# Optimization experiments

Hardware: AMD Instinct MI355X
Metric: run time of the kernel (lower is better)

Reference implementation:

```python
import jax, jax.numpy as jnp
import numpy as np

HEADS = 8
DIM_HEAD = 64
QUERY_DIM = 512
CONTEXT_DIM = 768
INNER_DIM = HEADS * DIM_HEAD  # 512
SCALE = DIM_HEAD ** -0.5


def setup_inputs() -> dict:
    key = jax.random.key(0)
    ks = jax.random.split(key, 7)
    B, N, M = 4, 2048, 1024
    x = jax.random.normal(ks[0], (B, N, QUERY_DIM), dtype=jnp.float32)
    context = jax.random.normal(ks[1], (B, M, CONTEXT_DIM), dtype=jnp.float32)
    # torch Linear weights stored as (out_features, in_features); y = x @ W.T
    Wq = jax.random.normal(ks[2], (INNER_DIM, QUERY_DIM), dtype=jnp.float32) * (QUERY_DIM ** -0.5)
    Wk = jax.random.normal(ks[3], (INNER_DIM, CONTEXT_DIM), dtype=jnp.float32) * (CONTEXT_DIM ** -0.5)
    Wv = jax.random.normal(ks[4], (INNER_DIM, CONTEXT_DIM), dtype=jnp.float32) * (CONTEXT_DIM ** -0.5)
    Wo = jax.random.normal(ks[5], (QUERY_DIM, INNER_DIM), dtype=jnp.float32) * (INNER_DIM ** -0.5)
    bo = jax.random.normal(ks[6], (QUERY_DIM,), dtype=jnp.float32) * 0.01
    return {"x": x, "context": context, "Wq": Wq, "Wk": Wk, "Wv": Wv, "Wo": Wo, "bo": bo}


def reference(x, context, Wq, Wk, Wv, Wo, bo):
    B, N, _ = x.shape
    M = context.shape[1]
    h, d = HEADS, DIM_HEAD
    q = jnp.einsum('bnc,ic->bni', x, Wq)        # [B,N,inner]
    k = jnp.einsum('bmc,ic->bmi', context, Wk)  # [B,M,inner]
    v = jnp.einsum('bmc,ic->bmi', context, Wv)  # [B,M,inner]
    # split heads: b n (h d) -> b h n d
    q = q.reshape(B, N, h, d).transpose(0, 2, 1, 3)
    k = k.reshape(B, M, h, d).transpose(0, 2, 1, 3)
    v = v.reshape(B, M, h, d).transpose(0, 2, 1, 3)
    # fp32 upcast for QK^T (inputs already fp32; kept explicit for fidelity)
    sim = jnp.einsum('bhnd,bhmd->bhnm', q.astype(jnp.float32), k.astype(jnp.float32)) * SCALE
    attn = jax.nn.softmax(sim, axis=-1)
    out = jnp.einsum('bhnm,bhmd->bhnd', attn, v)  # [B,h,N,d]
    out = out.transpose(0, 2, 1, 3).reshape(B, N, h * d)  # b n (h d)
    return jnp.einsum('bni,oi->bno', out, Wo) + bo  # dropout p=0 in eval
```

## Files before the change

### kernel.cpp

```cpp
#include <hip/hip_runtime.h>

using u16 = unsigned short;
typedef __bf16 bf16x8 __attribute__((ext_vector_type(8)));
typedef __bf16 bf16x2 __attribute__((ext_vector_type(2)));
typedef float  f32x4  __attribute__((ext_vector_type(4)));
typedef float  f32x16 __attribute__((ext_vector_type(16)));

#define MFMA16x16x32 __builtin_amdgcn_mfma_f32_16x16x32_bf16
#define MFMA32x32x16 __builtin_amdgcn_mfma_f32_32x32x16_bf16

#if __has_builtin(__builtin_amdgcn_exp2f)
#define EXP2 __builtin_amdgcn_exp2f
#else
#define EXP2 exp2f
#endif

static __device__ __forceinline__ unsigned f2bf_u(float f){
  unsigned x = __builtin_bit_cast(unsigned, f);
  return (x + 0x7fffu + ((x >> 16) & 1u)) >> 16;
}

static __device__ __forceinline__ void gll16(const void* g, void* l){
  __builtin_amdgcn_global_load_lds((const __attribute__((address_space(1))) void*)g,
                                   (__attribute__((address_space(3))) void*)l, 16, 0, 0);
}

static __device__ __forceinline__ f32x16 splat16(float x){
  f32x16 v;
#pragma unroll
  for (int i = 0; i < 16; ++i) v[i] = x;
  return v;
}

__global__ void __launch_bounds__(256) cvt_all(
    const float* __restrict__ x,  u16* __restrict__ xb,
    const float* __restrict__ cx, u16* __restrict__ cxb,
    const float* __restrict__ wq, u16* __restrict__ wqb,
    const float* __restrict__ wk, u16* __restrict__ wkb,
    const float* __restrict__ wv, u16* __restrict__ wvb,
    const float* __restrict__ wo, u16* __restrict__ wob)
{
  const float* in; u16* out; int n4;
  switch (blockIdx.y){
    case 0: in=x;  out=xb;  n4=(4*2048*512)/4; break;
    case 1: in=cx; out=cxb; n4=(4*1024*768)/4; break;
    case 2: in=wq; out=wqb; n4=(512*512)/4;    break;
    case 3: in=wk; out=wkb; n4=(512*768)/4;    break;
    case 4: in=wv; out=wvb; n4=(512*768)/4;    break;
    default:in=wo; out=wob; n4=(512*512)/4;    break;
  }
  int i = blockIdx.x*256 + threadIdx.x;
  const int stride = gridDim.x*256;
  for (; i < n4; i += stride){
    float4 f = ((const float4*)in)[i];
    ushort4 u;
    u.x = (u16)f2bf_u(f.x); u.y = (u16)f2bf_u(f.y);
    u.z = (u16)f2bf_u(f.z); u.w = (u16)f2bf_u(f.w);
    ((ushort4*)out)[i] = u;
  }
}

template<int LDA, int LDB, int KK, int OM>
static __device__ __forceinline__ void gemm_tile64(
    const u16* __restrict__ Ap, const u16* __restrict__ Bp,
    void* __restrict__ Cv, int ldc, int bx, int by,
    const float* __restrict__ bias, float scale,
    u16* __restrict__ sAp, u16* __restrict__ sBp)
{
  const int tid = threadIdx.x;
  const int w = tid >> 6, lane = tid & 63;
  const int wr = w >> 1, wc = w & 1;
  const long tm = (long)bx * 128;
  const long tn = (long)by * 64;

  f32x4 acc[4][2] = {};

  const int srl = lane >> 3, scc = lane & 7;

  auto stage = [&](int kt, int bb){
#pragma unroll
    for (int i = 0; i < 4; ++i){
      const int row = w*32 + i*8 + srl;
      const int sw = scc ^ (row & 7);
      gll16(Ap + (tm + row)*LDA + kt*64 + sw*8, sAp + bb*(128*64) + (w*32 + i*8)*64);
    }
#pragma unroll
    for (int i = 0; i < 2; ++i){
      const int row = w*16 + i*8 + srl;
      const int sw = scc ^ (row & 7);
      gll16(Bp + (tn + row)*LDB + kt*64 + sw*8, sBp + bb*(64*64) + (w*16 + i*8)*64);
    }
  };

  const int fr = lane & 15, fg = lane >> 4;
  constexpr int NK = KK / 64;

  stage(0, 0);
  __syncthreads();
  for (int kt = 0; kt < NK; ++kt){
    if (kt + 1 < NK) stage(kt + 1, (kt + 1) & 1);
    const int bb = kt & 1;
    bf16x8 af[4][2], bfr[2][2];
#pragma unroll
    for (int fm = 0; fm < 4; ++fm){
      const int row = wr*64 + fm*16 + fr;
      const int swz = row & 7;
#pragma unroll
      for (int s = 0; s < 2; ++s)
        af[fm][s] = *(const bf16x8*)&sAp[bb*(128*64) + row*64 + ((s*4 + fg) ^ swz)*8];
    }
#pragma unroll
    for (int fn = 0; fn < 2; ++fn){
      const int row = wc*32 + fn*16 + fr;
      const int swz = row & 7;
#pragma unroll
      for (int s = 0; s < 2; ++s)
        bfr[fn][s] = *(const bf16x8*)&sBp[bb*(64*64) + row*64 + ((s*4 + fg) ^ swz)*8];
    }
#pragma unroll
    for (int s = 0; s < 2; ++s)
#pragma unroll
      for (int fm = 0; fm < 4; ++fm)
#pragma unroll
        for (int fn = 0; fn < 2; ++fn)
          acc[fm][fn] = MFMA16x16x32(af[fm][s], bfr[fn][s], acc[fm][fn], 0, 0, 0);
    __syncthreads();
  }

#pragma unroll
  for (int fm = 0; fm < 4; ++fm){
#pragma unroll
    for (int fn = 0; fn < 2; ++fn){
      const long row0 = tm + wr*64 + fm*16 + fg*4;
      const long col  = tn + wc*32 + fn*16 + fr;
      if (OM == 0){
        u16* C = (u16*)Cv;
#pragma unroll
        for (int rr = 0; rr < 4; ++rr)
          C[(row0 + rr)*ldc + col] = (u16)f2bf_u(acc[fm][fn][rr] * scale);
      } else {
        float* C = (float*)Cv;
        const float bv = bias[col];
#pragma unroll
        for (int rr = 0; rr < 4; ++rr)
          C[(row0 + rr)*ldc + col] = acc[fm][fn][rr] + bv;
      }
    }
  }
}

template<int LDA, int LDB, int KK, int OM>
static __device__ __forceinline__ void gemm_tile128(
    const u16* __restrict__ Ap, const u16* __restrict__ Bp,
    void* __restrict__ Cv, int ldc, int bx, int by,
    const float* __restrict__ bias, float scale,
    u16* __restrict__ sAp, u16* __restrict__ sBp)
{
  const int tid = threadIdx.x;
  const int w = tid >> 6, lane = tid & 63;
  const int wr = w >> 1, wc = w & 1;
  const long tm = (long)bx * 128;
  const long tn = (long)by * 128;

  f32x4 acc[4][4] = {};

  const int srl = lane >> 3, scc = lane & 7;

  auto stage = [&](int kt, int bb){
#pragma unroll
    for (int i = 0; i < 4; ++i){
      const int row = w*32 + i*8 + srl;
      const int sw = scc ^ (row & 7);
      gll16(Ap + (tm + row)*LDA + kt*64 + sw*8, sAp + bb*(128*64) + (w*32 + i*8)*64);
      gll16(Bp + (tn + row)*LDB + kt*64 + sw*8, sBp + bb*(128*64) + (w*32 + i*8)*64);
    }
  };

  const int fr = lane & 15, fg = lane >> 4;
  constexpr int NK = KK / 64;

  stage(0, 0);
  __syncthreads();
  for (int kt = 0; kt < NK; ++kt){
    if (kt + 1 < NK) stage(kt + 1, (kt + 1) & 1);
    const int bb = kt & 1;
    bf16x8 af[4][2], bfr[4][2];
#pragma unroll
    for (int fm = 0; fm < 4; ++fm){
      const int row = wr*64 + fm*16 + fr;
      const int swz = row & 7;
#pragma unroll
      for (int s = 0; s < 2; ++s)
        af[fm][s] = *(const bf16x8*)&sAp[bb*(128*64) + row*64 + ((s*4 + fg) ^ swz)*8];
    }
#pragma unroll
    for (int fn = 0; fn < 4; ++fn){
      const int row = wc*64 + fn*16 + fr;
      const int swz = row & 7;
#pragma unroll
      for (int s = 0; s < 2; ++s)
        bfr[fn][s] = *(const bf16x8*)&sBp[bb*(128*64) + row*64 + ((s*4 + fg) ^ swz)*8];
    }
#pragma unroll
    for (int s = 0; s < 2; ++s)
#pragma unroll
      for (int fm = 0; fm < 4; ++fm)
#pragma unroll
        for (int fn = 0; fn < 4; ++fn)
          acc[fm][fn] = MFMA16x16x32(af[fm][s], bfr[fn][s], acc[fm][fn], 0, 0, 0);
    __syncthreads();
  }

#pragma unroll
  for (int fm = 0; fm < 4; ++fm){
#pragma unroll
    for (int fn = 0; fn < 4; ++fn){
      const long row0 = tm + wr*64 + fm*16 + fg*4;
      const long col  = tn + wc*64 + fn*16 + fr;
      if (OM == 0){
        u16* C = (u16*)Cv;
#pragma unroll
        for (int rr = 0; rr < 4; ++rr)
          C[(row0 + rr)*ldc + col] = (u16)f2bf_u(acc[fm][fn][rr] * scale);
      } else {
        float* C = (float*)Cv;
        const float bv = bias[col];
#pragma unroll
        for (int rr = 0; rr < 4; ++rr)
          C[(row0 + rr)*ldc + col] = acc[fm][fn][rr] + bv;
      }
    }
  }
}

__global__ __launch_bounds__(256, 2) void proj_fused(
    const u16* __restrict__ xb,  const u16* __restrict__ cxb,
    const u16* __restrict__ wqb, const u16* __restrict__ wkb,
    const u16* __restrict__ wvb,
    u16* __restrict__ qb, u16* __restrict__ kb, u16* __restrict__ vtb,
    float qscale)
{
  __shared__ u16 sA[2*128*64];
  __shared__ u16 sB[2*128*64];
  const int bid = blockIdx.x;
  const int lid = (bid & 7)*64 + (bid >> 3);
  if (lid < 256){
    gemm_tile128<512,512,512,0>(xb, wqb, (void*)qb, 512, lid >> 2, lid & 3,
                                nullptr, qscale, sA, sB);
  } else if (lid < 384){
    const int t = lid - 256;
    gemm_tile128<768,768,768,0>(cxb, wkb, (void*)kb, 512, t >> 2, t & 3,
                                nullptr, 1.0f, sA, sB);
  } else {
    const int t = lid - 384, z = t >> 5, r = t & 31;
    gemm_tile128<768,768,768,0>(wvb, cxb + (long)z*1024*768,
                                (void*)(vtb + (long)z*512*1024), 1024,
                                r >> 3, r & 7, nullptr, 1.0f, sA, sB);
  }
}

__global__ __launch_bounds__(256, 3) void gemm_out(
    const u16* __restrict__ ab, const u16* __restrict__ wob,
    float* __restrict__ out, const float* __restrict__ bias)
{
  __shared__ u16 sA[2*128*64];
  __shared__ u16 sB[2*64*64];
  const int bid = blockIdx.x;
  const int lid = (bid & 7)*64 + (bid >> 3);
  gemm_tile64<512,512,512,1>(ab, wob, (void*)out, 512, lid >> 3, lid & 7,
                             bias, 1.0f, sA, sB);
}

__global__ __launch_bounds__(512, 2) void attn_fwd(
    const u16* __restrict__ Q,
    const u16* __restrict__ Kb,
    const u16* __restrict__ Vt,
    u16* __restrict__ O)
{
  const int bid = blockIdx.x;
  const int lid = (bid & 7)*32 + (bid >> 3);
  const int qx = lid & 7, hh = (lid >> 3) & 7, b = lid >> 6;
  const int w = threadIdx.x >> 6, lane = threadIdx.x & 63;
  const int q31 = lane & 31, hi = lane >> 5;
  const int w4 = w & 3, kvg = w >> 2;
  const int q0 = qx*256 + w4*64;

  __shared__ u16 sAll[8][8192];
  __shared__ float sLsP[16*32];
  __shared__ float sLsT[8*32];

  bf16x8 qf[2][4];
#pragma unroll
  for (int j = 0; j < 2; ++j){
    const u16* qrow = Q + (long)(b*2048 + q0 + j*32 + q31)*512 + hh*64;
#pragma unroll
    for (int ks = 0; ks < 4; ++ks)
      qf[j][ks] = *(const bf16x8*)(qrow + ks*16 + hi*8);
  }

  f32x16 o[2][2] = {{splat16(0.f), splat16(0.f)}, {splat16(0.f), splat16(0.f)}};
  float lsum0 = 0.f, lsum1 = 0.f;

  const int srl = lane >> 3, scc = lane & 7;
  const int vr4 = lane >> 4, vc16 = lane & 15;

  auto stage = [&](int t){
    const int tv = 2*t + kvg;
    const int sl = t & 1;
#pragma unroll
    for (int i = 0; i < 4; ++i){
      const int row = w4*32 + i*8 + srl;
      const int cs = scc ^ (row & 7);
      gll16(Kb + (long)(b*1024 + tv*128 + row)*512 + hh*64 + cs*8,
            &sAll[kvg*2 + sl][(w4*32 + i*8)*64]);
    }
#pragma unroll
    for (int i = 0; i < 4; ++i){
      const int d = w4*16 + i*4 + vr4;
      const int cs = vc16 ^ (d & 15);
      gll16(Vt + (long)(b*512 + hh*64 + d)*1024 + tv*128 + cs*8,
            &sAll[4 + kvg*2 + sl][(w4*16 + i*4)*128]);
    }
  };

  stage(0);

  for (int t = 0; t < 4; ++t){
    asm volatile("s_waitcnt vmcnt(0)" ::: "memory");
    __builtin_amdgcn_s_barrier();
    asm volatile("" ::: "memory");
    if (t + 1 < 4) stage(t + 1);

    const u16* sKp = sAll[kvg*2 + (t & 1)];
    const u16* sVp = sAll[4 + kvg*2 + (t & 1)];

#pragma unroll
    for (int mt = 0; mt < 4; ++mt){
      f32x16 s0 = splat16(-16.f), s1 = splat16(-16.f);
      const int row = mt*32 + q31;
      const int swz = row & 7;
      __builtin_amdgcn_s_setprio(1);
#pragma unroll
      for (int ks = 0; ks < 4; ++ks){
        bf16x8 kf = *(const bf16x8*)&sKp[row*64 + ((ks*2 + hi) ^ swz)*8];
        s0 = MFMA32x32x16(kf, qf[0][ks], s0, 0, 0, 0);
        s1 = MFMA32x32x16(kf, qf[1][ks], s1, 0, 0, 0);
      }
      __builtin_amdgcn_s_setprio(0);

#pragma unroll
      for (int r = 0; r < 16; ++r) s0[r] = EXP2(s0[r]);
#pragma unroll
      for (int r = 0; r < 16; ++r) s1[r] = EXP2(s1[r]);
      {
        float a0=s0[0]+s0[1], a1=s0[2]+s0[3], a2=s0[4]+s0[5], a3=s0[6]+s0[7];
        float a4=s0[8]+s0[9], a5=s0[10]+s0[11], a6=s0[12]+s0[13], a7=s0[14]+s0[15];
        lsum0 += ((a0+a1)+(a2+a3)) + ((a4+a5)+(a6+a7));
        float c0=s1[0]+s1[1], c1=s1[2]+s1[3], c2=s1[4]+s1[5], c3=s1[6]+s1[7];
        float c4=s1[8]+s1[9], c5=s1[10]+s1[11], c6=s1[12]+s1[13], c7=s1[14]+s1[15];
        lsum1 += ((c0+c1)+(c2+c3)) + ((c4+c5)+(c6+c7));
      }
      unsigned pk0[8], pk1[8];
#pragma unroll
      for (int p2 = 0; p2 < 8; ++p2){
        union { bf16x2 h; unsigned u; } t0, t1;
        t0.h[0] = (__bf16)s0[2*p2]; t0.h[1] = (__bf16)s0[2*p2 + 1]; pk0[p2] = t0.u;
        t1.h[0] = (__bf16)s1[2*p2]; t1.h[1] = (__bf16)s1[2*p2 + 1]; pk1[p2] = t1.u;
      }

#pragma unroll
      for (int sl2 = 0; sl2 < 2; ++sl2){
        union { unsigned u[4]; bf16x8 v; } pa0, pa1;
        {
          unsigned a = pk0[sl2*4 + 0], bq = pk0[sl2*4 + 2];
          asm volatile("v_permlane32_swap_b32 %0, %1" : "+v"(a), "+v"(bq));
          pa0.u[0] = a;  pa0.u[2] = bq;
          unsigned a2 = pk0[sl2*4 + 1], b2 = pk0[sl2*4 + 3];
          asm volatile("v_permlane32_swap_b32 %0, %1" : "+v"(a2), "+v"(b2));
          pa0.u[1] = a2; pa0.u[3] = b2;
        }
        {
          unsigned a = pk1[sl2*4 + 0], bq = pk1[sl2*4 + 2];
          asm volatile("v_permlane32_swap_b32 %0, %1" : "+v"(a), "+v"(bq));
          pa1.u[0] = a;  pa1.u[2] = bq;
          unsigned a2 = pk1[sl2*4 + 1], b2 = pk1[sl2*4 + 3];
          asm volatile("v_permlane32_swap_b32 %0, %1" : "+v"(a2), "+v"(b2));
          pa1.u[1] = a2; pa1.u[3] = b2;
        }
        const int s = mt*2 + sl2;
        __builtin_amdgcn_s_setprio(1);
#pragma unroll
        for (int fd = 0; fd < 2; ++fd){
          const int vrow = fd*32 + q31;
          bf16x8 bv = *(const bf16x8*)&sVp[vrow*128 + (((s*2 + hi) ^ (vrow & 15)))*8];
          o[0][fd] = MFMA32x32x16(pa0.v, bv, o[0][fd], 0, 0, 0);
          o[1][fd] = MFMA32x32x16(pa1.v, bv, o[1][fd], 0, 0, 0);
        }
        __builtin_amdgcn_s_setprio(0);
      }
    }
    asm volatile("" ::: "memory");
  }

  lsum0 += __shfl_xor(lsum0, 32);
  lsum1 += __shfl_xor(lsum1, 32);
  sLsP[(w*2 + 0)*32 + q31] = lsum0;
  sLsP[(w*2 + 1)*32 + q31] = lsum1;
  __syncthreads();

  float* sO = (float*)&sAll[0][0];
  if (w >= 4){
#pragma unroll
    for (int j = 0; j < 2; ++j){
#pragma unroll
      for (int fd = 0; fd < 2; ++fd){
        float* p = sO + ((((w - 4)*2 + j)*2 + fd)*64*20) + lane*20;
#pragma unroll
        for (int k = 0; k < 4; ++k){
          f32x4 t4;
#pragma unroll
          for (int e = 0; e < 4; ++e) t4[e] = o[j][fd][4*k + e];
          *(f32x4*)(p + 4*k) = t4;
        }
      }
    }
  }
  __syncthreads();

  if (w < 4){
#pragma unroll
    for (int j = 0; j < 2; ++j){
#pragma unroll
      for (int fd = 0; fd < 2; ++fd){
        const float* p = sO + (((w*2 + j)*2 + fd)*64*20) + lane*20;
#pragma unroll
        for (int k = 0; k < 4; ++k){
          f32x4 t4 = *(const f32x4*)(p + 4*k);
#pragma unroll
          for (int e = 0; e < 4; ++e) o[j][fd][4*k + e] += t4[e];
        }
      }
    }
    const float lt0 = lsum0 + sLsP[((w + 4)*2 + 0)*32 + q31];
    const float lt1 = lsum1 + sLsP[((w + 4)*2 + 1)*32 + q31];
    sLsT[(w*2 + 0)*32 + q31] = lt0;
    sLsT[(w*2 + 1)*32 + q31] = lt1;
  }
  __syncthreads();

  if (w < 4){
#pragma unroll
    for (int j = 0; j < 2; ++j){
      f32x4 inv[4];
#pragma unroll
      for (int g = 0; g < 4; ++g){
        f32x4 ls = *(const f32x4*)&sLsT[(w*2 + j)*32 + 8*g + 4*hi];
#pragma unroll
        for (int e = 0; e < 4; ++e) inv[g][e] = 1.0f / ls[e];
      }
      u16* orow = O + (long)(b*2048 + q0 + j*32)*512 + hh*64;
#pragma unroll
      for (int fd = 0; fd < 2; ++fd){
#pragma unroll
        for (int r = 0; r < 16; ++r){
          const int q = (r & 3) + 8*(r >> 2) + 4*hi;
          const float val = o[j][fd][r] * inv[r >> 2][r & 3];
          orow[(long)q*512 + fd*32 + q31] = (u16)f2bf_u(val);
        }
      }
    }
  }
}

extern "C" void kernel_launch(void* const* d_in, const int* in_sizes, int n_in,
                              void* d_out, int out_size, void* d_ws, size_t ws_size,
                              hipStream_t stream)
{
  (void)in_sizes; (void)n_in; (void)out_size; (void)ws_size;
  const float* x   = (const float*)d_in[0];
  const float* ctx = (const float*)d_in[1];
  const float* Wq  = (const float*)d_in[2];
  const float* Wk  = (const float*)d_in[3];
  const float* Wv  = (const float*)d_in[4];
  const float* Wo  = (const float*)d_in[5];
  const float* bo  = (const float*)d_in[6];
  float* out = (float*)d_out;

  char* ws = (char*)d_ws;
  u16* xb  = (u16*)(ws + 0);
  u16* cxb = (u16*)(ws + 8388608);
  u16* wqb = (u16*)(ws + 14680064);
  u16* wkb = (u16*)(ws + 15204352);
  u16* wvb = (u16*)(ws + 15990784);
  u16* wob = (u16*)(ws + 16777216);
  u16* qb  = (u16*)(ws + 17301504);
  u16* kb  = (u16*)(ws + 25690112);
  u16* vtb = (u16*)(ws + 29884416);
  u16* ab  = (u16*)(ws + 34078720);

  cvt_all<<<dim3(1024, 6, 1), 256, 0, stream>>>(x, xb, ctx, cxb, Wq, wqb,
                                                Wk, wkb, Wv, wvb, Wo, wob);

  proj_fused<<<dim3(512, 1, 1), 256, 0, stream>>>(
      xb, cxb, wqb, wkb, wvb, qb, kb, vtb, 0.18033688011112042f);

  attn_fwd<<<dim3(256, 1, 1), 512, 0, stream>>>(qb, kb, vtb, ab);

  gemm_out<<<dim3(512, 1, 1), 256, 0, stream>>>(ab, wob, out, bo);
}
```

Before: 66.82 us.

## Write K/V in MFMA-fragment order and load attention operands directly from global

The K and V projection epilogues now scatter their outputs into a pre-swizzled layout that matches the per-lane MFMA operand order. The attention kernel then reads K and V fragments straight from global memory into registers with coalesced 16-byte loads, with no LDS staging, barriers or double buffering. This removes LDS traffic and synchronisation in the attention loop. In exchange it gives up cross-wave data sharing through LDS, so every wave reissues its own global or L2 loads and memory latency is exposed to the MFMA chain. The projection stores also become scattered.

```diff
diff --git a/kernel.cpp b/kernel.cpp
--- a/kernel.cpp
+++ b/kernel.cpp
@@ -222,12 +222,37 @@
 #pragma unroll
         for (int rr = 0; rr < 4; ++rr)
           C[(row0 + rr)*ldc + col] = (u16)f2bf_u(acc[fm][fn][rr] * scale);
-      } else {
+      } else if (OM == 1){
         float* C = (float*)Cv;
         const float bv = bias[col];
 #pragma unroll
         for (int rr = 0; rr < 4; ++rr)
           C[(row0 + rr)*ldc + col] = acc[fm][fn][rr] + bv;
+      } else if (OM == 2){
+        u16* C = (u16*)Cv;
+        const int hh2 = (int)(col >> 6), d = (int)(col & 63);
+        const int ks = d >> 4, hi2 = (d >> 3) & 1, e = d & 7;
+#pragma unroll
+        for (int rr = 0; rr < 4; ++rr){
+          const long r = row0 + rr;
+          const int b2 = (int)(r >> 10), m = (int)(r & 1023);
+          const int tv = m >> 7, mtq = (m >> 5) & 3, q31r = m & 31;
+          const long off = ((long)((((b2*8 + hh2)*8 + tv)*4 + mtq)*4 + ks))*512
+                         + (hi2*32 + q31r)*8 + e;
+          C[off] = (u16)f2bf_u(acc[fm][fn][rr] * scale);
+        }
+      } else {
+        u16* C = (u16*)Cv;
+        const int m = (int)col;
+        const int tv = m >> 7, s = (m >> 4) & 7, hi2 = (m >> 3) & 1, e = m & 7;
+#pragma unroll
+        for (int rr = 0; rr < 4; ++rr){
+          const int i = (int)(row0 + rr);
+          const int hh2 = i >> 6, d0 = i & 63, fd = d0 >> 5, q31v = d0 & 31;
+          const long off = ((long)((((hh2*8 + tv)*8 + s)*2 + fd)*2 + hi2))*256
+                         + q31v*8 + e;
+          C[off] = (u16)f2bf_u(acc[fm][fn][rr] * scale);
+        }
       }
     }
   }
@@ -237,7 +262,7 @@
     const u16* __restrict__ xb,  const u16* __restrict__ cxb,
     const u16* __restrict__ wqb, const u16* __restrict__ wkb,
     const u16* __restrict__ wvb,
-    u16* __restrict__ qb, u16* __restrict__ kb, u16* __restrict__ vtb,
+    u16* __restrict__ qb, u16* __restrict__ kpb, u16* __restrict__ vpb,
     float qscale)
 {
   __shared__ u16 sA[2*128*64];
@@ -249,12 +274,12 @@
                                 nullptr, qscale, sA, sB);
   } else if (lid < 384){
     const int t = lid - 256;
-    gemm_tile128<768,768,768,0>(cxb, wkb, (void*)kb, 512, t >> 2, t & 3,
+    gemm_tile128<768,768,768,2>(cxb, wkb, (void*)kpb, 0, t >> 2, t & 3,
                                 nullptr, 1.0f, sA, sB);
   } else {
     const int t = lid - 384, z = t >> 5, r = t & 31;
-    gemm_tile128<768,768,768,0>(wvb, cxb + (long)z*1024*768,
-                                (void*)(vtb + (long)z*512*1024), 1024,
+    gemm_tile128<768,768,768,3>(wvb, cxb + (long)z*1024*768,
+                                (void*)(vpb + (long)z*524288), 0,
                                 r >> 3, r & 7, nullptr, 1.0f, sA, sB);
   }
 }
@@ -273,8 +298,8 @@
 
 __global__ __launch_bounds__(512, 2) void attn_fwd(
     const u16* __restrict__ Q,
-    const u16* __restrict__ Kb,
-    const u16* __restrict__ Vt,
+    const u16* __restrict__ Kp,
+    const u16* __restrict__ Vp,
     u16* __restrict__ O)
 {
   const int bid = blockIdx.x;
@@ -284,11 +309,15 @@
   const int q31 = lane & 31, hi = lane >> 5;
   const int w4 = w & 3, kvg = w >> 2;
   const int q0 = qx*256 + w4*64;
-
-  __shared__ u16 sAll[8][8192];
+  const int bh = b*8 + hh;
+
+  __shared__ float sO[4*2*2*1280];
   __shared__ float sLsP[16*32];
   __shared__ float sLsT[8*32];
 
+  const u16* Kb2 = Kp + (long)bh*65536 + lane*8;
+  const u16* Vb2 = Vp + (long)bh*65536 + lane*8;
+
   bf16x8 qf[2][4];
 #pragma unroll
   for (int j = 0; j < 2; ++j){
@@ -301,105 +330,81 @@
   f32x16 o[2][2] = {{splat16(0.f), splat16(0.f)}, {splat16(0.f), splat16(0.f)}};
   float lsum0 = 0.f, lsum1 = 0.f;
 
-  const int srl = lane >> 3, scc = lane & 7;
-  const int vr4 = lane >> 4, vc16 = lane & 15;
-
-  auto stage = [&](int t){
-    const int tv = 2*t + kvg;
-    const int sl = t & 1;
-#pragma unroll
-    for (int i = 0; i < 4; ++i){
-      const int row = w4*32 + i*8 + srl;
-      const int cs = scc ^ (row & 7);
-      gll16(Kb + (long)(b*1024 + tv*128 + row)*512 + hh*64 + cs*8,
-            &sAll[kvg*2 + sl][(w4*32 + i*8)*64]);
-    }
-#pragma unroll
-    for (int i = 0; i < 4; ++i){
-      const int d = w4*16 + i*4 + vr4;
-      const int cs = vc16 ^ (d & 15);
-      gll16(Vt + (long)(b*512 + hh*64 + d)*1024 + tv*128 + cs*8,
-            &sAll[4 + kvg*2 + sl][(w4*16 + i*4)*128]);
-    }
-  };
-
-  stage(0);
-
-  for (int t = 0; t < 4; ++t){
-    asm volatile("s_waitcnt vmcnt(0)" ::: "memory");
-    __builtin_amdgcn_s_barrier();
-    asm volatile("" ::: "memory");
-    if (t + 1 < 4) stage(t + 1);
-
-    const u16* sKp = sAll[kvg*2 + (t & 1)];
-    const u16* sVp = sAll[4 + kvg*2 + (t & 1)];
-
-#pragma unroll
-    for (int mt = 0; mt < 4; ++mt){
-      f32x16 s0 = splat16(-16.f), s1 = splat16(-16.f);
-      const int row = mt*32 + q31;
-      const int swz = row & 7;
+#pragma unroll 2
+  for (int u = 0; u < 16; ++u){
+    const int tv = kvg*4 + (u >> 2);
+    const int mt = u & 3;
+    const u16* kp = Kb2 + (long)((tv*4 + mt)*4)*512;
+    bf16x8 kf0 = *(const bf16x8*)(kp);
+    bf16x8 kf1 = *(const bf16x8*)(kp + 512);
+    bf16x8 kf2 = *(const bf16x8*)(kp + 1024);
+    bf16x8 kf3 = *(const bf16x8*)(kp + 1536);
+    const u16* vp = Vb2 + (long)((tv*8 + mt*2)*2)*512;
+    bf16x8 bv00 = *(const bf16x8*)(vp);
+    bf16x8 bv01 = *(const bf16x8*)(vp + 512);
+    bf16x8 bv10 = *(const bf16x8*)(vp + 1024);
+    bf16x8 bv11 = *(const bf16x8*)(vp + 1536);
+
+    f32x16 s0 = splat16(-16.f), s1 = splat16(-16.f);
+    __builtin_amdgcn_s_setprio(1);
+    s0 = MFMA32x32x16(kf0, qf[0][0], s0, 0, 0, 0);
+    s1 = MFMA32x32x16(kf0, qf[1][0], s1, 0, 0, 0);
+    s0 = MFMA32x32x16(kf1, qf[0][1], s0, 0, 0, 0);
+    s1 = MFMA32x32x16(kf1, qf[1][1], s1, 0, 0, 0);
+    s0 = MFMA32x32x16(kf2, qf[0][2], s0, 0, 0, 0);
+    s1 = MFMA32x32x16(kf2, qf[1][2], s1, 0, 0, 0);
+    s0 = MFMA32x32x16(kf3, qf[0][3], s0, 0, 0, 0);
+    s1 = MFMA32x32x16(kf3, qf[1][3], s1, 0, 0, 0);
+    __builtin_amdgcn_s_setprio(0);
+
+#pragma unroll
+    for (int r = 0; r < 16; ++r) s0[r] = EXP2(s0[r]);
+#pragma unroll
+    for (int r = 0; r < 16; ++r) s1[r] = EXP2(s1[r]);
+    {
+      float a0=s0[0]+s0[1], a1=s0[2]+s0[3], a2=s0[4]+s0[5], a3=s0[6]+s0[7];
+      float a4=s0[8]+s0[9], a5=s0[10]+s0[11], a6=s0[12]+s0[13], a7=s0[14]+s0[15];
+      lsum0 += ((a0+a1)+(a2+a3)) + ((a4+a5)+(a6+a7));
+      float c0=s1[0]+s1[1], c1=s1[2]+s1[3], c2=s1[4]+s1[5], c3=s1[6]+s1[7];
+      float c4=s1[8]+s1[9], c5=s1[10]+s1[11], c6=s1[12]+s1[13], c7=s1[14]+s1[15];
+      lsum1 += ((c0+c1)+(c2+c3)) + ((c4+c5)+(c6+c7));
+    }
+    unsigned pk0[8], pk1[8];
+#pragma unroll
+    for (int p2 = 0; p2 < 8; ++p2){
+      union { bf16x2 h; unsigned u; } t0, t1;
+      t0.h[0] = (__bf16)s0[2*p2]; t0.h[1] = (__bf16)s0[2*p2 + 1]; pk0[p2] = t0.u;
+      t1.h[0] = (__bf16)s1[2*p2]; t1.h[1] = (__bf16)s1[2*p2 + 1]; pk1[p2] = t1.u;
+    }
+
+#pragma unroll
+    for (int sl2 = 0; sl2 < 2; ++sl2){
+      union { unsigned u[4]; bf16x8 v; } pa0, pa1;
+      {
+        unsigned a = pk0[sl2*4 + 0], bq = pk0[sl2*4 + 2];
+        asm volatile("v_permlane32_swap_b32 %0, %1" : "+v"(a), "+v"(bq));
+        pa0.u[0] = a;  pa0.u[2] = bq;
+        unsigned a2 = pk0[sl2*4 + 1], b2 = pk0[sl2*4 + 3];
+        asm volatile("v_permlane32_swap_b32 %0, %1" : "+v"(a2), "+v"(b2));
+        pa0.u[1] = a2; pa0.u[3] = b2;
+      }
+      {
+        unsigned a = pk1[sl2*4 + 0], bq = pk1[sl2*4 + 2];
+        asm volatile("v_permlane32_swap_b32 %0, %1" : "+v"(a), "+v"(bq));
+        pa1.u[0] = a;  pa1.u[2] = bq;
+        unsigned a2 = pk1[sl2*4 + 1], b2 = pk1[sl2*4 + 3];
+        asm volatile("v_permlane32_swap_b32 %0, %1" : "+v"(a2), "+v"(b2));
+        pa1.u[1] = a2; pa1.u[3] = b2;
+      }
+      const bf16x8 bvf0 = sl2 ? bv10 : bv00;
+      const bf16x8 bvf1 = sl2 ? bv11 : bv01;
       __builtin_amdgcn_s_setprio(1);
-#pragma unroll
-      for (int ks = 0; ks < 4; ++ks){
-        bf16x8 kf = *(const bf16x8*)&sKp[row*64 + ((ks*2 + hi) ^ swz)*8];
-        s0 = MFMA32x32x16(kf, qf[0][ks], s0, 0, 0, 0);
-        s1 = MFMA32x32x16(kf, qf[1][ks], s1, 0, 0, 0);
-      }
+      o[0][0] = MFMA32x32x16(pa0.v, bvf0, o[0][0], 0, 0, 0);
+      o[1][0] = MFMA32x32x16(pa1.v, bvf0, o[1][0], 0, 0, 0);
+      o[0][1] = MFMA32x32x16(pa0.v, bvf1, o[0][1], 0, 0, 0);
+      o[1][1] = MFMA32x32x16(pa1.v, bvf1, o[1][1], 0, 0, 0);
       __builtin_amdgcn_s_setprio(0);
-
-#pragma unroll
-      for (int r = 0; r < 16; ++r) s0[r] = EXP2(s0[r]);
-#pragma unroll
-      for (int r = 0; r < 16; ++r) s1[r] = EXP2(s1[r]);
-      {
-        float a0=s0[0]+s0[1], a1=s0[2]+s0[3], a2=s0[4]+s0[5], a3=s0[6]+s0[7];
-        float a4=s0[8]+s0[9], a5=s0[10]+s0[11], a6=s0[12]+s0[13], a7=s0[14]+s0[15];
-        lsum0 += ((a0+a1)+(a2+a3)) + ((a4+a5)+(a6+a7));
-        float c0=s1[0]+s1[1], c1=s1[2]+s1[3], c2=s1[4]+s1[5], c3=s1[6]+s1[7];
-        float c4=s1[8]+s1[9], c5=s1[10]+s1[11], c6=s1[12]+s1[13], c7=s1[14]+s1[15];
-        lsum1 += ((c0+c1)+(c2+c3)) + ((c4+c5)+(c6+c7));
-      }
-      unsigned pk0[8], pk1[8];
-#pragma unroll
-      for (int p2 = 0; p2 < 8; ++p2){
-        union { bf16x2 h; unsigned u; } t0, t1;
-        t0.h[0] = (__bf16)s0[2*p2]; t0.h[1] = (__bf16)s0[2*p2 + 1]; pk0[p2] = t0.u;
-        t1.h[0] = (__bf16)s1[2*p2]; t1.h[1] = (__bf16)s1[2*p2 + 1]; pk1[p2] = t1.u;
-      }
-
-#pragma unroll
-      for (int sl2 = 0; sl2 < 2; ++sl2){
-        union { unsigned u[4]; bf16x8 v; } pa0, pa1;
-        {
-          unsigned a = pk0[sl2*4 + 0], bq = pk0[sl2*4 + 2];
-          asm volatile("v_permlane32_swap_b32 %0, %1" : "+v"(a), "+v"(bq));
-          pa0.u[0] = a;  pa0.u[2] = bq;
-          unsigned a2 = pk0[sl2*4 + 1], b2 = pk0[sl2*4 + 3];
-          asm volatile("v_permlane32_swap_b32 %0, %1" : "+v"(a2), "+v"(b2));
-          pa0.u[1] = a2; pa0.u[3] = b2;
-        }
-        {
-          unsigned a = pk1[sl2*4 + 0], bq = pk1[sl2*4 + 2];
-          asm volatile("v_permlane32_swap_b32 %0, %1" : "+v"(a), "+v"(bq));
-          pa1.u[0] = a;  pa1.u[2] = bq;
-          unsigned a2 = pk1[sl2*4 + 1], b2 = pk1[sl2*4 + 3];
-          asm volatile("v_permlane32_swap_b32 %0, %1" : "+v"(a2), "+v"(b2));
-          pa1.u[1] = a2; pa1.u[3] = b2;
-        }
-        const int s = mt*2 + sl2;
-        __builtin_amdgcn_s_setprio(1);
-#pragma unroll
-        for (int fd = 0; fd < 2; ++fd){
-          const int vrow = fd*32 + q31;
-          bf16x8 bv = *(const bf16x8*)&sVp[vrow*128 + (((s*2 + hi) ^ (vrow & 15)))*8];
-          o[0][fd] = MFMA32x32x16(pa0.v, bv, o[0][fd], 0, 0, 0);
-          o[1][fd] = MFMA32x32x16(pa1.v, bv, o[1][fd], 0, 0, 0);
-        }
-        __builtin_amdgcn_s_setprio(0);
-      }
-    }
-    asm volatile("" ::: "memory");
+    }
   }
 
   lsum0 += __shfl_xor(lsum0, 32);
@@ -408,13 +413,12 @@
   sLsP[(w*2 + 1)*32 + q31] = lsum1;
   __syncthreads();
 
-  float* sO = (float*)&sAll[0][0];
   if (w >= 4){
 #pragma unroll
     for (int j = 0; j < 2; ++j){
 #pragma unroll
       for (int fd = 0; fd < 2; ++fd){
-        float* p = sO + ((((w - 4)*2 + j)*2 + fd)*64*20) + lane*20;
+        float* p = sO + ((((w - 4)*2 + j)*2 + fd)*1280) + lane*20;
 #pragma unroll
         for (int k = 0; k < 4; ++k){
           f32x4 t4;
@@ -432,7 +436,7 @@
     for (int j = 0; j < 2; ++j){
 #pragma unroll
       for (int fd = 0; fd < 2; ++fd){
-        const float* p = sO + (((w*2 + j)*2 + fd)*64*20) + lane*20;
+        const float* p = sO + (((w*2 + j)*2 + fd)*1280) + lane*20;
 #pragma unroll
         for (int k = 0; k < 4; ++k){
           f32x4 t4 = *(const f32x4*)(p + 4*k);
@@ -494,17 +498,17 @@
   u16* wvb = (u16*)(ws + 15990784);
   u16* wob = (u16*)(ws + 16777216);
   u16* qb  = (u16*)(ws + 17301504);
-  u16* kb  = (u16*)(ws + 25690112);
-  u16* vtb = (u16*)(ws + 29884416);
+  u16* kpb = (u16*)(ws + 25690112);
+  u16* vpb = (u16*)(ws + 29884416);
   u16* ab  = (u16*)(ws + 34078720);
 
   cvt_all<<<dim3(1024, 6, 1), 256, 0, stream>>>(x, xb, ctx, cxb, Wq, wqb,
                                                 Wk, wkb, Wv, wvb, Wo, wob);
 
   proj_fused<<<dim3(512, 1, 1), 256, 0, stream>>>(
-      xb, cxb, wqb, wkb, wvb, qb, kb, vtb, 0.18033688011112042f);
-
-  attn_fwd<<<dim3(256, 1, 1), 512, 0, stream>>>(qb, kb, vtb, ab);
+      xb, cxb, wqb, wkb, wvb, qb, kpb, vpb, 0.18033688011112042f);
+
+  attn_fwd<<<dim3(256, 1, 1), 512, 0, stream>>>(qb, kpb, vpb, ab);
 
   gemm_out<<<dim3(512, 1, 1), 256, 0, stream>>>(ab, wob, out, bo);
 }
```

After: 68.60 us. +2.7%, slower.
